# Performance work log

Hardware: AMD Instinct MI355X
Metric: run time of the kernel (lower is better)

The kernel has to match this reference:

```python
import jax, jax.numpy as jnp
import numpy as np

N_AGENT = 60000
N_MAP = 40000
N = N_AGENT + N_MAP
E = 3200000
HID = 32
PERIODS = 30
PRED = 50


def setup_inputs() -> dict:
    key = jax.random.key(0)
    ks = jax.random.split(key, 20)
    def w(k, shape, s=0.1):
        return jax.random.normal(k, shape, jnp.float32) * s
    return {
        "agent_x": jax.random.normal(ks[0], (N_AGENT, 9), jnp.float32),
        "map_x": jax.random.normal(ks[1], (N_MAP, 6), jnp.float32),
        "edge_index": jax.random.randint(ks[2], (2, E), 0, N),
        "W_agent": w(ks[3], (9, HID)), "b_agent": jnp.zeros((HID,), jnp.float32),
        "W_map": w(ks[4], (6, HID)), "b_map": jnp.zeros((HID,), jnp.float32),
        # TGCN cell: three GCNConvs (z, r, h gates) + three Linear(2*HID -> HID)
        "Wz_c": w(ks[5], (HID, HID)), "bz_c": jnp.zeros((HID,), jnp.float32),
        "Wr_c": w(ks[6], (HID, HID)), "br_c": jnp.zeros((HID,), jnp.float32),
        "Wh_c": w(ks[7], (HID, HID)), "bh_c": jnp.zeros((HID,), jnp.float32),
        "Wz_l": w(ks[8], (2 * HID, HID)), "bz_l": jnp.zeros((HID,), jnp.float32),
        "Wr_l": w(ks[9], (2 * HID, HID)), "br_l": jnp.zeros((HID,), jnp.float32),
        "Wh_l": w(ks[10], (2 * HID, HID)), "bh_l": jnp.zeros((HID,), jnp.float32),
        "attn": w(ks[11], (PERIODS,), 1.0),
        "W1": w(ks[12], (HID, 2 * HID)), "b1": jnp.zeros((2 * HID,), jnp.float32),
        "W2": w(ks[13], (2 * HID, 2 * PRED)), "b2": jnp.zeros((2 * PRED,), jnp.float32),
    }


def reference(agent_x, map_x, edge_index, W_agent, b_agent, W_map, b_map,
              Wz_c, bz_c, Wr_c, br_c, Wh_c, bh_c,
              Wz_l, bz_l, Wr_l, br_l, Wh_l, bh_l,
              attn, W1, b1, W2, b2):
    n = agent_x.shape[0] + map_x.shape[0]
    # encoders + concat map nodes after agent nodes
    x = jnp.concatenate([agent_x @ W_agent + b_agent,
                         map_x @ W_map + b_map], axis=0)  # [N, HID]

    # GCN normalization with self-loops: A_hat = D^-1/2 (A + I) D^-1/2
    loop = jnp.arange(n, dtype=edge_index.dtype)
    src = jnp.concatenate([edge_index[0], loop])
    dst = jnp.concatenate([edge_index[1], loop])
    deg = jax.ops.segment_sum(jnp.ones(src.shape[0], jnp.float32), dst, num_segments=n)
    dinv = jnp.where(deg > 0, jax.lax.rsqrt(deg), 0.0)
    norm = dinv[src] * dinv[dst]  # [E + N]

    def gcn(W, b):
        m = (x @ W)[src] * norm[:, None]          # gather + scale: [E+N, HID]
        return jax.ops.segment_sum(m, dst, num_segments=n) + b

    zeros_h = jnp.zeros_like(x)  # hidden state H = 0 (A3TGCN never threads H)
    z = jax.nn.sigmoid(jnp.concatenate([gcn(Wz_c, bz_c), zeros_h], 1) @ Wz_l + bz_l)
    r = jax.nn.sigmoid(jnp.concatenate([gcn(Wr_c, br_c), zeros_h], 1) @ Wr_l + br_l)
    h_tilde = jnp.tanh(jnp.concatenate([gcn(Wh_c, bh_c), zeros_h * r], 1) @ Wh_l + bh_l)
    h_new = (1.0 - z) * h_tilde  # z*H + (1-z)*h_tilde with H=0

    # attention-weighted sum over periods; every period is identical so it
    # collapses to sum(softmax(attn)) * h_new (== h_new, kept for fidelity)
    probs = jax.nn.softmax(attn)
    h_acc = jnp.sum(probs) * h_new

    h = jax.nn.relu(h_acc)[:agent_x.shape[0]]     # keep agent nodes only
    pred = jax.nn.relu(h @ W1 + b1) @ W2 + b2     # [num_agents, 2*PRED]
    return pred.reshape(-1, PRED, 2)
```

## Files before the change

### kernel.cpp

```cpp
#include <hip/hip_runtime.h>
#include <hip/hip_fp16.h>
#include <math.h>

#define N_AGENT 60000
#define N_MAP   40000
#define N_NODES 100000
#define NE      3200000
#define HID     32
#define PERIODS 30

#define NBUCK   391
#define NABUCK  235
#define CAP     10240
#define TILE    4096
#define PTHREADS 512
#define ABLK    128

#define BUFSZ   10724
#define OF_MZ   0
#define OF_MH   1024
#define OF_W1   2048
#define OF_W2   4096
#define OF_BZ   10496
#define OF_BH   10528
#define OF_B1   10560
#define OF_B2   10624

__global__ void k_precompute(const float* Wz_c, const float* bz_c,
                             const float* Wh_c, const float* bh_c,
                             const float* Wz_l, const float* bz_l,
                             const float* Wh_l, const float* bh_l,
                             const float* attn,
                             float* Mz, float* Mh, float* bz_eff, float* bh_eff,
                             float* s_out, int* cursor) {
    int t = threadIdx.x;
    int k = t >> 5, c = t & 31;
    float mz = 0.f, mh = 0.f;
    for (int j = 0; j < HID; ++j) {
        mz += Wz_c[k * HID + j] * Wz_l[j * HID + c];
        mh += Wh_c[k * HID + j] * Wh_l[j * HID + c];
    }
    Mz[t] = mz; Mh[t] = mh;
    if (t < NBUCK) cursor[t] = t * CAP;
    if (t < HID) {
        float bz = bz_l[t], bh = bh_l[t];
        for (int j = 0; j < HID; ++j) {
            bz += bz_c[j] * Wz_l[j * HID + t];
            bh += bh_c[j] * Wh_l[j * HID + t];
        }
        bz_eff[t] = bz; bh_eff[t] = bh;
    }
    if (t == 0) {
        float m = -1e30f;
        for (int i = 0; i < PERIODS; ++i) m = fmaxf(m, attn[i]);
        float S = 0.f;
        for (int i = 0; i < PERIODS; ++i) S += expf(attn[i] - m);
        float s = 0.f;
        for (int i = 0; i < PERIODS; ++i) s += expf(attn[i] - m) / S;
        *s_out = s;
    }
}

__global__ __launch_bounds__(PTHREADS) void k_partition(
        const int* __restrict__ src, const int* __restrict__ dst,
        int* __restrict__ cursor, int* __restrict__ ebuf) {
    __shared__ int sCnt[NBUCK];
    __shared__ int sBase[NBUCK + 1];
    __shared__ int sGbase[NBUCK];
    __shared__ int sScan[PTHREADS];
    __shared__ int sReorder[TILE];
    int t = threadIdx.x;
    int tileBase = blockIdx.x * TILE;
    int tcount = NE - tileBase; if (tcount > TILE) tcount = TILE;

    if (t < NBUCK) sCnt[t] = 0;
    __syncthreads();

    int pb[8], pp[8], pr[8];
    const int4* s4 = (const int4*)src;
    const int4* d4 = (const int4*)dst;
#pragma unroll
    for (int k = 0; k < 2; ++k) {
        int e4 = (tileBase >> 2) + t + k * PTHREADS;
        int valid = (e4 << 2) < NE;
        int4 sv, dv;
        if (valid) { sv = s4[e4]; dv = d4[e4]; }
#define PROC(m, SS, DD) { int kk = k * 4 + m;                                  \
        if (valid) { pb[kk] = (DD) >> 8;                                       \
                     pp[kk] = (SS) | (((DD) & 255) << 17);                     \
                     pr[kk] = atomicAdd(&sCnt[pb[kk]], 1); }                   \
        else pb[kk] = -1; }
        PROC(0, sv.x, dv.x)
        PROC(1, sv.y, dv.y)
        PROC(2, sv.z, dv.z)
        PROC(3, sv.w, dv.w)
#undef PROC
    }
    __syncthreads();

    int v = (t < NBUCK) ? sCnt[t] : 0;
    sScan[t] = v;
    __syncthreads();
    for (int s = 1; s < PTHREADS; s <<= 1) {
        int a = (t >= s) ? sScan[t - s] : 0;
        __syncthreads();
        sScan[t] += a;
        __syncthreads();
    }
    if (t <= NBUCK) sBase[t] = sScan[t] - v;
    __syncthreads();
    if (t < NBUCK && sCnt[t] > 0) sGbase[t] = atomicAdd(&cursor[t], sCnt[t]);
    __syncthreads();
#pragma unroll
    for (int k = 0; k < 8; ++k) {
        if (pb[k] >= 0) sReorder[sBase[pb[k]] + pr[k]] = pp[k];
    }
    __syncthreads();
#pragma unroll
    for (int k = 0; k < 8; ++k) {
        int j = t + k * PTHREADS;
        if (j < tcount) {
            int lo = 0, hi = NBUCK;
            while (hi - lo > 1) {
                int m = (lo + hi) >> 1;
                if (sBase[m] <= j) lo = m; else hi = m;
            }
            ebuf[sGbase[lo] + (j - sBase[lo])] = sReorder[j];
        }
    }
}

__global__ __launch_bounds__(256) void k_hist(const int* __restrict__ cursor,
                                              const int* __restrict__ ebuf,
                                              int* __restrict__ deg,
                                              int* __restrict__ qdeg) {
    __shared__ int h[1024];
    int t = threadIdx.x;
    int b = blockIdx.x;
    for (int j = t; j < 1024; j += 256) h[j] = 0;
    __syncthreads();
    int start = b * CAP;
    int cnt = cursor[b] - start;
    for (int j = t; j < cnt; j += 256) {
        int p = ebuf[start + j];
        int dl = (p >> 17) & 255;
        int s = p & 0x1FFFF;
        int qt = (s >= 25000) + (s >= 50000) + (s >= 75000);
        atomicAdd(&h[dl * 4 + qt], 1);
    }
    __syncthreads();
    int node = b * 256 + t;
    if (node < N_NODES)
        deg[node] = h[t * 4] + h[t * 4 + 1] + h[t * 4 + 2] + h[t * 4 + 3];
    for (int j = t; j < 1024; j += 256) {
        int q4 = b * 1024 + j;
        if (q4 < N_NODES * 4) qdeg[q4] = h[j];
    }
}

__global__ void k_encode(const float* __restrict__ agent_x, const float* __restrict__ map_x,
                         const float* __restrict__ W_agent, const float* __restrict__ b_agent,
                         const float* __restrict__ W_map, const float* __restrict__ b_map,
                         const int* __restrict__ deg,
                         __half* __restrict__ y_h) {
    int t = blockIdx.x * blockDim.x + threadIdx.x;
    if (t >= (N_NODES + 1) * HID) return;
    int i = t >> 5, c = t & 31;
    float acc = 0.f;
    if (i < N_AGENT) {
        float v = (c < 9) ? agent_x[(size_t)i * 9 + c] : 0.f;
        acc = b_agent[c];
#pragma unroll
        for (int k = 0; k < 9; ++k) acc += __shfl(v, k, 32) * W_agent[k * HID + c];
        acc *= rsqrtf((float)deg[i] + 1.0f);
    } else if (i < N_NODES) {
        float v = (c < 6) ? map_x[(size_t)(i - N_AGENT) * 6 + c] : 0.f;
        acc = b_map[c];
#pragma unroll
        for (int k = 0; k < 6; ++k) acc += __shfl(v, k, 32) * W_map[k * HID + c];
        acc *= rsqrtf((float)deg[i] + 1.0f);
    }
    y_h[t] = __float2half(acc);
}

__global__ __launch_bounds__(1024) void k_sortlocal(
        const int* __restrict__ cursor, int* __restrict__ ebuf,
        const int* __restrict__ qdeg, int* __restrict__ row_start) {
    __shared__ int sSorted[CAP];
    __shared__ int sBase[1024];
    __shared__ int sCnt[1024];
    __shared__ int sScan[1024];
    int t = threadIdx.x;
    const int b = blockIdx.x;

    int v = qdeg[b * 1024 + t];
    sCnt[t] = 0;
    sScan[t] = v;
    __syncthreads();
    for (int st = 1; st < 1024; st <<= 1) {
        int a = (t >= st) ? sScan[t - st] : 0;
        __syncthreads();
        sScan[t] += a;
        __syncthreads();
    }
    sBase[t] = sScan[t] - v;
    if ((t & 3) == 0) row_start[b * 256 + (t >> 2)] = b * CAP + sBase[t];
    __syncthreads();

    const int start = b * CAP;
    const int cnt = cursor[b] - start;
    for (int j = t; j < cnt; j += 1024) {
        int p = ebuf[start + j];
        int dl = (p >> 17) & 255;
        int s = p & 0x1FFFF;
        int qt = (s >= 25000) + (s >= 50000) + (s >= 75000);
        int bin = dl * 4 + qt;
        int r = atomicAdd(&sCnt[bin], 1);
        sSorted[sBase[bin] + r] = s;
    }
    __syncthreads();
    for (int j = t; j < cnt; j += 1024)
        ebuf[start + j] = sSorted[j];
}

__global__ __launch_bounds__(1024) void k_aggmlp(
        const int* __restrict__ row_start, const int* __restrict__ deg,
        const int* __restrict__ ebuf, const __half* __restrict__ y_h,
        const float* __restrict__ Mz, const float* __restrict__ Mh,
        const float* __restrict__ bz_eff, const float* __restrict__ bh_eff,
        const float* __restrict__ s_ptr,
        const float* __restrict__ W1, const float* __restrict__ b1,
        const float* __restrict__ W2, const float* __restrict__ b2,
        float* __restrict__ out) {
    __shared__ float sBuf[BUFSZ];
    __shared__ float sAcc[ABLK * 32];
    __shared__ int   sOff[ABLK + 1];
    int t = threadIdx.x;
    const int nodeBase = blockIdx.x * ABLK;

    if (t < ABLK) sOff[t] = row_start[nodeBase + t];
    if (t == ABLK) {
        int last = nodeBase + ABLK - 1;
        sOff[ABLK] = row_start[last] + deg[last];
    }
    __syncthreads();

    int* sEdge = (int*)sBuf;
    const int e_begin = sOff[0];
    const int cnt = sOff[ABLK] - e_begin;
    for (int j = t; j < cnt; j += 1024) sEdge[j] = ebuf[e_begin + j];
    __syncthreads();

    const int lane = t & 63;
    const int r = (t >> 6) * 8 + (lane >> 3);
    const int q = lane & 7;
    const int i = nodeBase + r;
    const uint2* yh2 = (const uint2*)y_h;

    if (i < N_AGENT) {
        int e0 = sOff[r] - e_begin, e1 = sOff[r + 1] - e_begin;
        float ax = 0.f, ay = 0.f, az = 0.f, aw = 0.f;
        for (int j = e0; j < e1; j += 8) {
            uint2 v[8];
#pragma unroll
            for (int u = 0; u < 8; ++u) {
                int idx = (j + u < e1) ? sEdge[j + u] : N_NODES;
                v[u] = yh2[(size_t)idx * 8 + q];
            }
#pragma unroll
            for (int u = 0; u < 8; ++u) {
                __half2 h0 = *reinterpret_cast<__half2*>(&v[u].x);
                __half2 h1 = *reinterpret_cast<__half2*>(&v[u].y);
                float2 f0 = __half22float2(h0);
                float2 f1 = __half22float2(h1);
                ax += f0.x; ay += f0.y; az += f1.x; aw += f1.y;
            }
        }
        *(float4*)&sAcc[r * 32 + q * 4] = make_float4(ax, ay, az, aw);
    }
    __syncthreads();

    sBuf[OF_MZ + t] = Mz[t];
    sBuf[OF_MH + t] = Mh[t];
    for (int j = t; j < 2048; j += 1024) sBuf[OF_W1 + j] = W1[j];
    for (int j = t; j < 6400; j += 1024) sBuf[OF_W2 + j] = W2[j];
    if (t < 32) { sBuf[OF_BZ + t] = bz_eff[t]; sBuf[OF_BH + t] = bh_eff[t]; }
    if (t >= 64 && t < 128) sBuf[OF_B1 + t - 64] = b1[t - 64];
    if (t >= 128 && t < 228) sBuf[OF_B2 + t - 128] = b2[t - 128];
    __syncthreads();

    const float s = *s_ptr;
    const int c = t & 31, g2 = t >> 5;
    for (int rr = g2; rr < ABLK; rr += 32) {
        int ii = nodeBase + rr;
        if (ii >= N_AGENT) break;
        float di = rsqrtf((float)deg[ii] + 1.0f);
        float selfv = __half2float(y_h[(size_t)ii * HID + c]);
        float a = (sAcc[rr * 32 + c] + selfv) * di;
        float uz = sBuf[OF_BZ + c], uh = sBuf[OF_BH + c];
#pragma unroll
        for (int k = 0; k < 32; ++k) {
            float ak = __shfl(a, k, 32);
            uz += ak * sBuf[OF_MZ + k * 32 + c];
            uh += ak * sBuf[OF_MH + k * 32 + c];
        }
        float z = 1.0f / (1.0f + expf(-uz));
        float h = s * (1.0f - z) * tanhf(uh);
        h = fmaxf(h, 0.0f);
        float t0 = sBuf[OF_B1 + c], t1 = sBuf[OF_B1 + c + 32];
#pragma unroll
        for (int k = 0; k < 32; ++k) {
            float hk = __shfl(h, k, 32);
            t0 += hk * sBuf[OF_W1 + k * 64 + c];
            t1 += hk * sBuf[OF_W1 + k * 64 + c + 32];
        }
        t0 = fmaxf(t0, 0.0f); t1 = fmaxf(t1, 0.0f);
        int j3 = (c < 4) ? (c + 96) : 99;
        float o0 = sBuf[OF_B2 + c];
        float o1 = sBuf[OF_B2 + c + 32];
        float o2 = sBuf[OF_B2 + c + 64];
        float o3 = sBuf[OF_B2 + j3];
#pragma unroll
        for (int k = 0; k < 32; ++k) {
            float ta = __shfl(t0, k, 32);
            float tb = __shfl(t1, k, 32);
            o0 += ta * sBuf[OF_W2 + k * 100 + c]      + tb * sBuf[OF_W2 + (k + 32) * 100 + c];
            o1 += ta * sBuf[OF_W2 + k * 100 + c + 32] + tb * sBuf[OF_W2 + (k + 32) * 100 + c + 32];
            o2 += ta * sBuf[OF_W2 + k * 100 + c + 64] + tb * sBuf[OF_W2 + (k + 32) * 100 + c + 64];
            o3 += ta * sBuf[OF_W2 + k * 100 + j3]     + tb * sBuf[OF_W2 + (k + 32) * 100 + j3];
        }
        float* orow = out + (size_t)ii * 100;
        orow[c] = o0;
        orow[c + 32] = o1;
        orow[c + 64] = o2;
        if (c < 4) orow[c + 96] = o3;
    }
}

extern "C" void kernel_launch(void* const* d_in, const int* in_sizes, int n_in,
                              void* d_out, int out_size, void* d_ws, size_t ws_size,
                              hipStream_t stream) {
    const float* agent_x = (const float*)d_in[0];
    const float* map_x   = (const float*)d_in[1];
    const int*   ei      = (const int*)d_in[2];
    const float* W_agent = (const float*)d_in[3];
    const float* b_agent = (const float*)d_in[4];
    const float* W_map   = (const float*)d_in[5];
    const float* b_map   = (const float*)d_in[6];
    const float* Wz_c    = (const float*)d_in[7];
    const float* bz_c    = (const float*)d_in[8];
    const float* Wh_c    = (const float*)d_in[11];
    const float* bh_c    = (const float*)d_in[12];
    const float* Wz_l    = (const float*)d_in[13];
    const float* bz_l    = (const float*)d_in[14];
    const float* Wh_l    = (const float*)d_in[17];
    const float* bh_l    = (const float*)d_in[18];
    const float* attn    = (const float*)d_in[19];
    const float* W1      = (const float*)d_in[20];
    const float* b1      = (const float*)d_in[21];
    const float* W2      = (const float*)d_in[22];
    const float* b2      = (const float*)d_in[23];
    float* out = (float*)d_out;

    const int* e_src = ei;
    const int* e_dst = ei + NE;

    float*  ws       = (float*)d_ws;
    __half* y_h      = (__half*)ws;
    float*  Mz       = ws + 1600128;
    float*  Mh       = ws + 1601152;
    float*  bz       = ws + 1602176;
    float*  bh       = ws + 1602208;
    float*  sS       = ws + 1602240;
    int*    deg      = (int*)(ws + 1602304);
    int*    cursor   = (int*)(ws + 1702400);
    int*    row_start= (int*)(ws + 1702912);
    int*    qdeg     = (int*)(ws + 1763328);
    int*    ebuf     = (int*)(ws + 2163328);

    k_precompute<<<1, 1024, 0, stream>>>(Wz_c, bz_c, Wh_c, bh_c, Wz_l, bz_l,
                                         Wh_l, bh_l, attn, Mz, Mh, bz, bh, sS, cursor);
    k_partition<<<(NE + TILE - 1) / TILE, PTHREADS, 0, stream>>>(e_src, e_dst, cursor, ebuf);
    k_hist<<<NBUCK, 256, 0, stream>>>(cursor, ebuf, deg, qdeg);
    k_encode<<<((N_NODES + 1) * HID + 255) / 256, 256, 0, stream>>>(
        agent_x, map_x, W_agent, b_agent, W_map, b_map, deg, y_h);
    k_sortlocal<<<NABUCK, 1024, 0, stream>>>(cursor, ebuf, qdeg, row_start);
    k_aggmlp<<<(N_AGENT + ABLK - 1) / ABLK, 1024, 0, stream>>>(
        row_start, deg, ebuf, y_h, Mz, Mh, bz, bh, sS, W1, b1, W2, b2, out);
}
```

Baseline: 306.5 us.

## Split fused aggregation+MLP kernel into separate gather and per-thread MLP kernels

Splits the fused aggregation/MLP kernel into two kernels. The gather kernel now uses a smaller 32 KB shared edge buffer, with a global-memory fallback when a block has more edges than fit, and writes the pre-activation sums to a new global h_pre buffer. The new MLP kernel gives each thread one node and keeps activations in registers, reading the weights through uniform global loads instead of staging them in shared memory. This is meant to raise occupancy of the gather phase and remove the shuffle-heavy MLP. In exchange it adds an extra round trip of an N_AGENT x 32 float buffer, one more launch, heavy register pressure in the MLP, and uncoalesced 100-float row stores per thread.

```diff
diff --git a/kernel.cpp b/kernel.cpp
--- a/kernel.cpp
+++ b/kernel.cpp
@@ -15,16 +15,7 @@
 #define TILE    4096
 #define PTHREADS 512
 #define ABLK    128
-
-#define BUFSZ   10724
-#define OF_MZ   0
-#define OF_MH   1024
-#define OF_W1   2048
-#define OF_W2   4096
-#define OF_BZ   10496
-#define OF_BH   10528
-#define OF_B1   10560
-#define OF_B2   10624
+#define GEBLK   8192
 
 __global__ void k_precompute(const float* Wz_c, const float* bz_c,
                              const float* Wh_c, const float* bh_c,
@@ -223,117 +214,159 @@
         ebuf[start + j] = sSorted[j];
 }
 
-__global__ __launch_bounds__(1024) void k_aggmlp(
+__global__ __launch_bounds__(1024) void k_agg(
         const int* __restrict__ row_start, const int* __restrict__ deg,
         const int* __restrict__ ebuf, const __half* __restrict__ y_h,
+        float* __restrict__ h_pre) {
+    __shared__ int sEdge[GEBLK];
+    __shared__ int sOff[ABLK + 1];
+    int t = threadIdx.x;
+    const int nodeBase = blockIdx.x * ABLK;
+
+    if (t < ABLK) sOff[t] = row_start[nodeBase + t];
+    if (t == ABLK) {
+        int last = nodeBase + ABLK - 1;
+        sOff[ABLK] = row_start[last] + deg[last];
+    }
+    __syncthreads();
+
+    const int e_begin = sOff[0];
+    const int cnt = sOff[ABLK] - e_begin;
+    for (int j = t; j < cnt && j < GEBLK; j += 1024) sEdge[j] = ebuf[e_begin + j];
+    __syncthreads();
+
+    const int lane = t & 63;
+    const int r = (t >> 6) * 8 + (lane >> 3);
+    const int q = lane & 7;
+    const int i = nodeBase + r;
+    const uint2* yh2 = (const uint2*)y_h;
+
+    if (i < N_AGENT) {
+        float ax = 0.f, ay = 0.f, az = 0.f, aw = 0.f;
+        if (cnt <= GEBLK) {
+            int e0 = sOff[r] - e_begin, e1 = sOff[r + 1] - e_begin;
+            for (int j = e0; j < e1; j += 8) {
+                uint2 v[8];
+#pragma unroll
+                for (int u = 0; u < 8; ++u) {
+                    int idx = (j + u < e1) ? sEdge[j + u] : N_NODES;
+                    v[u] = yh2[(size_t)idx * 8 + q];
+                }
+#pragma unroll
+                for (int u = 0; u < 8; ++u) {
+                    __half2 h0 = *reinterpret_cast<__half2*>(&v[u].x);
+                    __half2 h1 = *reinterpret_cast<__half2*>(&v[u].y);
+                    float2 f0 = __half22float2(h0);
+                    float2 f1 = __half22float2(h1);
+                    ax += f0.x; ay += f0.y; az += f1.x; aw += f1.y;
+                }
+            }
+        } else {
+            int e0 = sOff[r], e1 = sOff[r + 1];
+            for (int j = e0; j < e1; j += 8) {
+                uint2 v[8];
+#pragma unroll
+                for (int u = 0; u < 8; ++u) {
+                    int idx = (j + u < e1) ? ebuf[j + u] : N_NODES;
+                    v[u] = yh2[(size_t)idx * 8 + q];
+                }
+#pragma unroll
+                for (int u = 0; u < 8; ++u) {
+                    __half2 h0 = *reinterpret_cast<__half2*>(&v[u].x);
+                    __half2 h1 = *reinterpret_cast<__half2*>(&v[u].y);
+                    float2 f0 = __half22float2(h0);
+                    float2 f1 = __half22float2(h1);
+                    ax += f0.x; ay += f0.y; az += f1.x; aw += f1.y;
+                }
+            }
+        }
+        *(float4*)&h_pre[(size_t)i * HID + q * 4] = make_float4(ax, ay, az, aw);
+    }
+}
+
+__global__ __launch_bounds__(256) void k_mlp(
+        const int* __restrict__ deg, const float* __restrict__ h_pre,
+        const __half* __restrict__ y_h,
         const float* __restrict__ Mz, const float* __restrict__ Mh,
         const float* __restrict__ bz_eff, const float* __restrict__ bh_eff,
         const float* __restrict__ s_ptr,
         const float* __restrict__ W1, const float* __restrict__ b1,
         const float* __restrict__ W2, const float* __restrict__ b2,
         float* __restrict__ out) {
-    __shared__ float sBuf[BUFSZ];
-    __shared__ float sAcc[ABLK * 32];
-    __shared__ int   sOff[ABLK + 1];
-    int t = threadIdx.x;
-    const int nodeBase = blockIdx.x * ABLK;
-
-    if (t < ABLK) sOff[t] = row_start[nodeBase + t];
-    if (t == ABLK) {
-        int last = nodeBase + ABLK - 1;
-        sOff[ABLK] = row_start[last] + deg[last];
-    }
-    __syncthreads();
-
-    int* sEdge = (int*)sBuf;
-    const int e_begin = sOff[0];
-    const int cnt = sOff[ABLK] - e_begin;
-    for (int j = t; j < cnt; j += 1024) sEdge[j] = ebuf[e_begin + j];
-    __syncthreads();
-
-    const int lane = t & 63;
-    const int r = (t >> 6) * 8 + (lane >> 3);
-    const int q = lane & 7;
-    const int i = nodeBase + r;
-    const uint2* yh2 = (const uint2*)y_h;
-
-    if (i < N_AGENT) {
-        int e0 = sOff[r] - e_begin, e1 = sOff[r + 1] - e_begin;
-        float ax = 0.f, ay = 0.f, az = 0.f, aw = 0.f;
-        for (int j = e0; j < e1; j += 8) {
-            uint2 v[8];
-#pragma unroll
-            for (int u = 0; u < 8; ++u) {
-                int idx = (j + u < e1) ? sEdge[j + u] : N_NODES;
-                v[u] = yh2[(size_t)idx * 8 + q];
+    int n = blockIdx.x * 256 + threadIdx.x;
+    if (n >= N_AGENT) return;
+    const float s = *s_ptr;
+    float di = rsqrtf((float)deg[n] + 1.0f);
+
+    float a[32];
+    const float4* hp4 = (const float4*)(h_pre + (size_t)n * HID);
+    const uint2*  sh2 = (const uint2*)(y_h + (size_t)n * HID);
+#pragma unroll
+    for (int u = 0; u < 8; ++u) {
+        float4 hv = hp4[u];
+        uint2 sv = sh2[u];
+        __half2 s0 = *reinterpret_cast<const __half2*>(&sv.x);
+        __half2 s1 = *reinterpret_cast<const __half2*>(&sv.y);
+        float2 f0 = __half22float2(s0);
+        float2 f1 = __half22float2(s1);
+        a[u * 4 + 0] = (hv.x + f0.x) * di;
+        a[u * 4 + 1] = (hv.y + f0.y) * di;
+        a[u * 4 + 2] = (hv.z + f1.x) * di;
+        a[u * 4 + 3] = (hv.w + f1.y) * di;
+    }
+
+    float hv32[32];
+#pragma unroll
+    for (int cc = 0; cc < 4; ++cc) {
+        float uz[8], uh[8];
+#pragma unroll
+        for (int j = 0; j < 8; ++j) { uz[j] = bz_eff[cc * 8 + j]; uh[j] = bh_eff[cc * 8 + j]; }
+#pragma unroll
+        for (int k = 0; k < 32; ++k) {
+#pragma unroll
+            for (int j = 0; j < 8; ++j) {
+                uz[j] += a[k] * Mz[k * 32 + cc * 8 + j];
+                uh[j] += a[k] * Mh[k * 32 + cc * 8 + j];
             }
-#pragma unroll
-            for (int u = 0; u < 8; ++u) {
-                __half2 h0 = *reinterpret_cast<__half2*>(&v[u].x);
-                __half2 h1 = *reinterpret_cast<__half2*>(&v[u].y);
-                float2 f0 = __half22float2(h0);
-                float2 f1 = __half22float2(h1);
-                ax += f0.x; ay += f0.y; az += f1.x; aw += f1.y;
-            }
-        }
-        *(float4*)&sAcc[r * 32 + q * 4] = make_float4(ax, ay, az, aw);
-    }
-    __syncthreads();
-
-    sBuf[OF_MZ + t] = Mz[t];
-    sBuf[OF_MH + t] = Mh[t];
-    for (int j = t; j < 2048; j += 1024) sBuf[OF_W1 + j] = W1[j];
-    for (int j = t; j < 6400; j += 1024) sBuf[OF_W2 + j] = W2[j];
-    if (t < 32) { sBuf[OF_BZ + t] = bz_eff[t]; sBuf[OF_BH + t] = bh_eff[t]; }
-    if (t >= 64 && t < 128) sBuf[OF_B1 + t - 64] = b1[t - 64];
-    if (t >= 128 && t < 228) sBuf[OF_B2 + t - 128] = b2[t - 128];
-    __syncthreads();
-
-    const float s = *s_ptr;
-    const int c = t & 31, g2 = t >> 5;
-    for (int rr = g2; rr < ABLK; rr += 32) {
-        int ii = nodeBase + rr;
-        if (ii >= N_AGENT) break;
-        float di = rsqrtf((float)deg[ii] + 1.0f);
-        float selfv = __half2float(y_h[(size_t)ii * HID + c]);
-        float a = (sAcc[rr * 32 + c] + selfv) * di;
-        float uz = sBuf[OF_BZ + c], uh = sBuf[OF_BH + c];
+        }
+#pragma unroll
+        for (int j = 0; j < 8; ++j) {
+            float z = 1.0f / (1.0f + expf(-uz[j]));
+            float hh = s * (1.0f - z) * tanhf(uh[j]);
+            hv32[cc * 8 + j] = fmaxf(hh, 0.0f);
+        }
+    }
+
+    float tv[64];
+#pragma unroll
+    for (int tc = 0; tc < 8; ++tc) {
+        float acc[8];
+#pragma unroll
+        for (int j = 0; j < 8; ++j) acc[j] = b1[tc * 8 + j];
 #pragma unroll
         for (int k = 0; k < 32; ++k) {
-            float ak = __shfl(a, k, 32);
-            uz += ak * sBuf[OF_MZ + k * 32 + c];
-            uh += ak * sBuf[OF_MH + k * 32 + c];
-        }
-        float z = 1.0f / (1.0f + expf(-uz));
-        float h = s * (1.0f - z) * tanhf(uh);
-        h = fmaxf(h, 0.0f);
-        float t0 = sBuf[OF_B1 + c], t1 = sBuf[OF_B1 + c + 32];
-#pragma unroll
-        for (int k = 0; k < 32; ++k) {
-            float hk = __shfl(h, k, 32);
-            t0 += hk * sBuf[OF_W1 + k * 64 + c];
-            t1 += hk * sBuf[OF_W1 + k * 64 + c + 32];
-        }
-        t0 = fmaxf(t0, 0.0f); t1 = fmaxf(t1, 0.0f);
-        int j3 = (c < 4) ? (c + 96) : 99;
-        float o0 = sBuf[OF_B2 + c];
-        float o1 = sBuf[OF_B2 + c + 32];
-        float o2 = sBuf[OF_B2 + c + 64];
-        float o3 = sBuf[OF_B2 + j3];
-#pragma unroll
-        for (int k = 0; k < 32; ++k) {
-            float ta = __shfl(t0, k, 32);
-            float tb = __shfl(t1, k, 32);
-            o0 += ta * sBuf[OF_W2 + k * 100 + c]      + tb * sBuf[OF_W2 + (k + 32) * 100 + c];
-            o1 += ta * sBuf[OF_W2 + k * 100 + c + 32] + tb * sBuf[OF_W2 + (k + 32) * 100 + c + 32];
-            o2 += ta * sBuf[OF_W2 + k * 100 + c + 64] + tb * sBuf[OF_W2 + (k + 32) * 100 + c + 64];
-            o3 += ta * sBuf[OF_W2 + k * 100 + j3]     + tb * sBuf[OF_W2 + (k + 32) * 100 + j3];
-        }
-        float* orow = out + (size_t)ii * 100;
-        orow[c] = o0;
-        orow[c + 32] = o1;
-        orow[c + 64] = o2;
-        if (c < 4) orow[c + 96] = o3;
+#pragma unroll
+            for (int j = 0; j < 8; ++j)
+                acc[j] += hv32[k] * W1[k * 64 + tc * 8 + j];
+        }
+#pragma unroll
+        for (int j = 0; j < 8; ++j) tv[tc * 8 + j] = fmaxf(acc[j], 0.0f);
+    }
+
+    float* orow = out + (size_t)n * 100;
+    for (int oc = 0; oc < 13; ++oc) {
+        int cbase = oc * 8; if (cbase > 92) cbase = 92;
+        float acc[8];
+#pragma unroll
+        for (int j = 0; j < 8; ++j) acc[j] = b2[cbase + j];
+#pragma unroll
+        for (int k = 0; k < 64; ++k) {
+#pragma unroll
+            for (int j = 0; j < 8; ++j)
+                acc[j] += tv[k] * W2[k * 100 + cbase + j];
+        }
+#pragma unroll
+        for (int j = 0; j < 8; ++j) orow[cbase + j] = acc[j];
     }
 }
 
@@ -376,7 +409,8 @@
     int*    cursor   = (int*)(ws + 1702400);
     int*    row_start= (int*)(ws + 1702912);
     int*    qdeg     = (int*)(ws + 1763328);
-    int*    ebuf     = (int*)(ws + 2163328);
+    float*  h_pre    = ws + 2163328;
+    int*    ebuf     = (int*)(ws + 4088448);
 
     k_precompute<<<1, 1024, 0, stream>>>(Wz_c, bz_c, Wh_c, bh_c, Wz_l, bz_l,
                                          Wh_l, bh_l, attn, Mz, Mh, bz, bh, sS, cursor);
@@ -385,6 +419,8 @@
     k_encode<<<((N_NODES + 1) * HID + 255) / 256, 256, 0, stream>>>(
         agent_x, map_x, W_agent, b_agent, W_map, b_map, deg, y_h);
     k_sortlocal<<<NABUCK, 1024, 0, stream>>>(cursor, ebuf, qdeg, row_start);
-    k_aggmlp<<<(N_AGENT + ABLK - 1) / ABLK, 1024, 0, stream>>>(
-        row_start, deg, ebuf, y_h, Mz, Mh, bz, bh, sS, W1, b1, W2, b2, out);
-}
+    k_agg<<<(N_AGENT + ABLK - 1) / ABLK, 1024, 0, stream>>>(
+        row_start, deg, ebuf, y_h, h_pre);
+    k_mlp<<<(N_AGENT + 255) / 256, 256, 0, stream>>>(
+        deg, h_pre, y_h, Mz, Mh, bz, bh, sS, W1, b1, W2, b2, out);
+}
```

Result: no change. 311.6 us (+1.7%).
